# Kernel optimization log

Measured on AMD Instinct MI355X. Metric: run time of the kernel, lower is better.

The kernel has to match this reference:

```python
import jax, jax.numpy as jnp
import numpy as np

C = 64      # extra_msa_channel
AC = 8      # attention_channel (per-head dim)
H = 8       # num_head
LN_EPS = 1e-5


def setup_inputs() -> dict:
    key = jax.random.key(0)
    ks = jax.random.split(key, 8)
    B, S, R = 1, 2048, 384
    msa_act = jax.random.normal(ks[0], (B, S, R, C), dtype=jnp.float32)
    msa_mask = jnp.ones((B, S, R), dtype=jnp.float32)
    # parameters (stored as [in, out] so x @ W matches torch Linear(x) = x @ W.T)
    sq = 1.0 / np.sqrt(C)
    wq = jax.random.normal(ks[1], (C, AC * H), dtype=jnp.float32) * sq
    wk = jax.random.normal(ks[2], (C, AC), dtype=jnp.float32) * sq
    wv = jax.random.normal(ks[3], (C, AC), dtype=jnp.float32) * sq
    wg = jax.random.normal(ks[4], (C, AC * H), dtype=jnp.float32) * sq
    bg = jnp.zeros((AC * H,), dtype=jnp.float32)
    wo = jax.random.normal(ks[5], (AC * H, C), dtype=jnp.float32) / np.sqrt(AC * H)
    bo = jnp.zeros((C,), dtype=jnp.float32)
    ln_scale = jnp.ones((C,), dtype=jnp.float32)
    ln_bias = jnp.zeros((C,), dtype=jnp.float32)
    return {"msa_act": msa_act, "msa_mask": msa_mask, "ln_scale": ln_scale,
            "ln_bias": ln_bias, "wq": wq, "wk": wk, "wv": wv, "wg": wg,
            "bg": bg, "wo": wo, "bo": bo}


def _layer_norm(x, scale, bias):
    mu = jnp.mean(x, axis=-1, keepdims=True)
    var = jnp.mean(jnp.square(x - mu), axis=-1, keepdims=True)
    return (x - mu) * jax.lax.rsqrt(var + LN_EPS) * scale + bias


def reference(msa_act, msa_mask, ln_scale, ln_bias, wq, wk, wv, wg, bg, wo, bo):
    # msa_act: [B, S, R, C] -> [B, R, S, C]; attention runs over S per column R
    act = jnp.swapaxes(msa_act, -2, -3)
    # msa_mask transposed in source but unused in the math
    act = _layer_norm(act, ln_scale, ln_bias)
    B, R, S, _ = act.shape
    # mean-pooled single query per column
    q_avg = jnp.mean(act, axis=-2)                       # [B, R, C]
    q = (q_avg @ wq).reshape(B, R, H, AC) * (AC ** -0.5)  # [B, R, H, ac]
    k = act @ wk                                          # [B, R, S, ac]
    v = act @ wv                                          # [B, R, S, ac]
    gate = jax.nn.sigmoid((act @ wg + bg).reshape(B, R, S, H, AC))
    logits = jnp.einsum('brhc,brsc->brhs', q, k)
    w = jax.nn.softmax(logits, axis=-1)                   # [B, R, H, S]
    out_1d = jnp.einsum('brhs,brsc->brhc', w, v)          # [B, R, H, ac]
    out_1d = out_1d[..., None, :, :] * gate               # [B, R, S, H, ac]
    out = out_1d.reshape(B, R, S, H * AC) @ wo + bo       # [B, R, S, C]
    return jnp.swapaxes(out, -2, -3)                      # [B, S, R, C]
```

## Files before the change

### kernel.cpp

```cpp
#include <hip/hip_runtime.h>

#define S_LEN 2048
#define R_LEN 384
#define C_DIM 64

typedef unsigned short u16;
typedef unsigned int u32;
typedef __attribute__((ext_vector_type(8))) short s8v;
typedef __attribute__((ext_vector_type(4))) float f4v;

__device__ __forceinline__ float bf2f(u16 h) {
    union { u32 u; float f; } c; c.u = ((u32)h) << 16; return c.f;
}
__device__ __forceinline__ u16 f2bf(float f) {
    union { float f; u32 u; } c; c.f = f;
    return (u16)((c.u + 0x7fffu + ((c.u >> 16) & 1u)) >> 16);
}
__device__ __forceinline__ void unpack8(uint4 q, float* o) {
    o[0] = bf2f((u16)(q.x & 0xffffu)); o[1] = bf2f((u16)(q.x >> 16));
    o[2] = bf2f((u16)(q.y & 0xffffu)); o[3] = bf2f((u16)(q.y >> 16));
    o[4] = bf2f((u16)(q.z & 0xffffu)); o[5] = bf2f((u16)(q.z >> 16));
    o[6] = bf2f((u16)(q.w & 0xffffu)); o[7] = bf2f((u16)(q.w >> 16));
}
__device__ __forceinline__ void split8(const float* y, uint4& qh, uint4& ql) {
    u16 h[8]; u16 l[8];
    #pragma unroll
    for (int j = 0; j < 8; ++j) {
        h[j] = f2bf(y[j]);
        l[j] = f2bf(y[j] - bf2f(h[j]));
    }
    qh.x = (u32)h[0] | ((u32)h[1] << 16); qh.y = (u32)h[2] | ((u32)h[3] << 16);
    qh.z = (u32)h[4] | ((u32)h[5] << 16); qh.w = (u32)h[6] | ((u32)h[7] << 16);
    ql.x = (u32)l[0] | ((u32)l[1] << 16); ql.y = (u32)l[2] | ((u32)l[3] << 16);
    ql.z = (u32)l[4] | ((u32)l[5] << 16); ql.w = (u32)l[6] | ((u32)l[7] << 16);
}
__device__ __forceinline__ void load8f(const float* p, float* o) {
    float4 a = *(const float4*)p;
    float4 b = *(const float4*)(p + 4);
    o[0] = a.x; o[1] = a.y; o[2] = a.z; o[3] = a.w;
    o[4] = b.x; o[5] = b.y; o[6] = b.z; o[7] = b.w;
}
#define XS_SWZ(row, bc) ((((int)(row)) << 7) + (((int)(bc)) ^ ((((int)(row)) & 7) << 4)))

__global__ __launch_bounds__(256) void k1_colattn(
    const float* __restrict__ act, const float* __restrict__ lnsp, const float* __restrict__ lnbp,
    const float* __restrict__ wq, const float* __restrict__ wk, const float* __restrict__ wv,
    float* __restrict__ o1g)
{
    __shared__ __align__(16) char smem[32768 + 32768 + 65536 + 8192 + 1024 + 512];
    char* xsh = smem;
    char* xsl = smem + 32768;
    char* kvb = smem + 65536;
    float* scrA = (float*)(smem + 131072);
    float* scrC = (float*)(smem + 139264);
    float* qavg = (float*)(smem + 140288);
    float* qlds = qavg + 64;

    const int t = threadIdx.x;
    const int r = blockIdx.x;
    const int lane = t & 63;
    const int w = t >> 6;
    const int grp = t & 7;
    const int rowb = t >> 3;
    const int n16 = lane & 15;
    const int kgrp = lane >> 4;

    float lns_r[8], lnb_r[8];
    load8f(lnsp + grp * 8, lns_r);
    load8f(lnbp + grp * 8, lnb_r);

    s8v bkv0, bkv1;
    {
        #pragma unroll
        for (int j = 0; j < 8; ++j) {
            int k0 = (kgrp << 3) + j;
            float e0 = (n16 < 8) ? wk[k0 * 8 + n16] : wv[k0 * 8 + (n16 - 8)];
            float e1 = (n16 < 8) ? wk[(k0 + 32) * 8 + n16] : wv[(k0 + 32) * 8 + (n16 - 8)];
            bkv0[j] = (short)f2bf(e0); bkv1[j] = (short)f2bf(e1);
        }
    }

    float qacc[8];
    #pragma unroll
    for (int j = 0; j < 8; ++j) qacc[j] = 0.f;

    for (int ci = 0; ci < 8; ++ci) {
        __syncthreads();
        #pragma unroll
        for (int sub = 0; sub < 8; ++sub) {
            int row = sub * 32 + rowb;
            int s = ci * 256 + row;
            float xf[8];
            load8f(act + ((size_t)s * R_LEN + r) * C_DIM + grp * 8, xf);
            float sum = 0.f, sq = 0.f;
            #pragma unroll
            for (int j = 0; j < 8; ++j) { sum += xf[j]; sq += xf[j] * xf[j]; }
            #pragma unroll
            for (int m = 1; m <= 4; m <<= 1) { sum += __shfl_xor(sum, m); sq += __shfl_xor(sq, m); }
            float mu = sum * (1.f / 64.f);
            float var = sq * (1.f / 64.f) - mu * mu;
            float rstd = rsqrtf(var + 1e-5f);
            float yv[8];
            #pragma unroll
            for (int j = 0; j < 8; ++j) {
                yv[j] = (xf[j] - mu) * rstd * lns_r[j] + lnb_r[j];
                qacc[j] += yv[j];
            }
            uint4 qh, ql; split8(yv, qh, ql);
            *(uint4*)(xsh + XS_SWZ(row, grp * 16)) = qh;
            *(uint4*)(xsl + XS_SWZ(row, grp * 16)) = ql;
        }
        __syncthreads();
        #pragma unroll
        for (int i4 = 0; i4 < 4; ++i4) {
            int tile = w * 4 + i4;
            s8v a0h = *(const s8v*)(xsh + XS_SWZ(tile * 16 + n16, kgrp * 16));
            s8v a1h = *(const s8v*)(xsh + XS_SWZ(tile * 16 + n16, 64 + kgrp * 16));
            s8v a0l = *(const s8v*)(xsl + XS_SWZ(tile * 16 + n16, kgrp * 16));
            s8v a1l = *(const s8v*)(xsl + XS_SWZ(tile * 16 + n16, 64 + kgrp * 16));
            f4v acc = {0.f, 0.f, 0.f, 0.f};
            acc = __builtin_amdgcn_mfma_f32_16x16x32_bf16(a0h, bkv0, acc, 0, 0, 0);
            acc = __builtin_amdgcn_mfma_f32_16x16x32_bf16(a1h, bkv1, acc, 0, 0, 0);
            acc = __builtin_amdgcn_mfma_f32_16x16x32_bf16(a0l, bkv0, acc, 0, 0, 0);
            acc = __builtin_amdgcn_mfma_f32_16x16x32_bf16(a1l, bkv1, acc, 0, 0, 0);
            #pragma unroll
            for (int jj = 0; jj < 4; ++jj) {
                int sg = ci * 256 + tile * 16 + kgrp * 4 + jj;
                int off = sg * 32 + ((n16 * 2) ^ (((sg >> 2) & 1) << 4));
                *(u16*)(kvb + off) = f2bf(acc[jj]);
            }
        }
    }

    #pragma unroll
    for (int j = 0; j < 8; ++j) scrA[t * 8 + j] = qacc[j];
    __syncthreads();
    if (t < 64) {
        float s = 0.f;
        for (int k = 0; k < 32; ++k) s += scrA[((t >> 3) + 8 * k) * 8 + (t & 7)];
        qavg[t] = s * (1.f / (float)S_LEN);
    }
    __syncthreads();
    if (t < 64) {
        float s = 0.f;
        for (int c = 0; c < 64; ++c) s += qavg[c] * wq[c * 64 + t];
        qlds[t] = s * 0.35355339059327373f;
    }
    __syncthreads();
    float q_r[64];
    #pragma unroll
    for (int c = 0; c < 64; ++c) q_r[c] = qlds[c];

    float mx[8];
    #pragma unroll
    for (int h = 0; h < 8; ++h) mx[h] = -1e30f;
    for (int i = 0; i < 8; ++i) {
        int s = i * 256 + t;
        int sw = ((s >> 2) & 1) << 4;
        float kf[8]; unpack8(*(const uint4*)(kvb + s * 32 + sw), kf);
        #pragma unroll
        for (int h = 0; h < 8; ++h) {
            float lg = 0.f;
            #pragma unroll
            for (int a = 0; a < 8; ++a) lg += q_r[h * 8 + a] * kf[a];
            mx[h] = fmaxf(mx[h], lg);
        }
    }
    #pragma unroll
    for (int h = 0; h < 8; ++h) scrA[t * 8 + h] = mx[h];
    __syncthreads();
    for (int st = 128; st >= 1; st >>= 1) {
        if (t < st) {
            #pragma unroll
            for (int h = 0; h < 8; ++h)
                scrA[t * 8 + h] = fmaxf(scrA[t * 8 + h], scrA[(t + st) * 8 + h]);
        }
        __syncthreads();
    }
    float mxf[8];
    #pragma unroll
    for (int h = 0; h < 8; ++h) mxf[h] = scrA[h];
    __syncthreads();

    float sm[8];
    float o1a[64];
    #pragma unroll
    for (int h = 0; h < 8; ++h) sm[h] = 0.f;
    #pragma unroll
    for (int e = 0; e < 64; ++e) o1a[e] = 0.f;
    for (int i = 0; i < 8; ++i) {
        int s = i * 256 + t;
        int sw = ((s >> 2) & 1) << 4;
        float kf[8]; unpack8(*(const uint4*)(kvb + s * 32 + sw), kf);
        float vf[8]; unpack8(*(const uint4*)(kvb + s * 32 + (16 ^ sw)), vf);
        #pragma unroll
        for (int h = 0; h < 8; ++h) {
            float lg = 0.f;
            #pragma unroll
            for (int a = 0; a < 8; ++a) lg += q_r[h * 8 + a] * kf[a];
            float p = __expf(lg - mxf[h]);
            sm[h] += p;
            #pragma unroll
            for (int a = 0; a < 8; ++a) o1a[h * 8 + a] += p * vf[a];
        }
    }
    #pragma unroll
    for (int h = 0; h < 8; ++h) scrA[t * 8 + h] = sm[h];
    __syncthreads();
    for (int st = 128; st >= 1; st >>= 1) {
        if (t < st) {
            #pragma unroll
            for (int h = 0; h < 8; ++h)
                scrA[t * 8 + h] += scrA[(t + st) * 8 + h];
        }
        __syncthreads();
    }
    #pragma unroll
    for (int m = 1; m < 64; m <<= 1) {
        #pragma unroll
        for (int e = 0; e < 64; ++e) o1a[e] += __shfl_xor(o1a[e], m);
    }
    #pragma unroll
    for (int e = 0; e < 64; ++e) if (lane == e) scrC[w * 64 + e] = o1a[e];
    __syncthreads();
    if (t < 64) {
        float v = scrC[t] + scrC[64 + t] + scrC[128 + t] + scrC[192 + t];
        float denom = scrA[t >> 3];
        o1g[r * 64 + t] = v / denom;
    }
}

__global__ __launch_bounds__(256) void k2_gateout(
    const float* __restrict__ act, const float* __restrict__ lnsp, const float* __restrict__ lnbp,
    const float* __restrict__ wg, const float* __restrict__ bgp,
    const float* __restrict__ wo, const float* __restrict__ bop,
    const float* __restrict__ o1g, float* __restrict__ out)
{
    __shared__ __align__(16) char bufH[32768];
    __shared__ __align__(16) char bufL[32768];
    const int t = threadIdx.x;
    const int r = blockIdx.x;
    const int s0 = blockIdx.y * 256;
    const int lane = t & 63;
    const int w = t >> 6;
    const int grp = t & 7;
    const int rowb = t >> 3;
    const int n16 = lane & 15;
    const int kgrp = lane >> 4;

    float lns_r[8], lnb_r[8];
    load8f(lnsp + grp * 8, lns_r);
    load8f(lnbp + grp * 8, lnb_r);

    float o1c[4], bgc[4], boc[4];
    #pragma unroll
    for (int c4 = 0; c4 < 4; ++c4) {
        int col = c4 * 16 + n16;
        o1c[c4] = o1g[r * 64 + col];
        bgc[c4] = bgp[col];
        boc[c4] = bop[col];
    }
    s8v wgf[4][2], wof[4][2];
    #pragma unroll
    for (int c4 = 0; c4 < 4; ++c4) {
        #pragma unroll
        for (int kb = 0; kb < 2; ++kb) {
            #pragma unroll
            for (int j = 0; j < 8; ++j) {
                int k = kb * 32 + kgrp * 8 + j;
                wgf[c4][kb][j] = (short)f2bf(wg[k * 64 + c4 * 16 + n16]);
                wof[c4][kb][j] = (short)f2bf(wo[k * 64 + c4 * 16 + n16]);
            }
        }
    }

    #pragma unroll
    for (int sub = 0; sub < 8; ++sub) {
        int row = sub * 32 + rowb;
        int s = s0 + row;
        float xf[8];
        load8f(act + ((size_t)s * R_LEN + r) * C_DIM + grp * 8, xf);
        float sum = 0.f, sq = 0.f;
        #pragma unroll
        for (int j = 0; j < 8; ++j) { sum += xf[j]; sq += xf[j] * xf[j]; }
        #pragma unroll
        for (int m = 1; m <= 4; m <<= 1) { sum += __shfl_xor(sum, m); sq += __shfl_xor(sq, m); }
        float mu = sum * (1.f / 64.f);
        float var = sq * (1.f / 64.f) - mu * mu;
        float rstd = rsqrtf(var + 1e-5f);
        float yv[8];
        #pragma unroll
        for (int j = 0; j < 8; ++j) yv[j] = (xf[j] - mu) * rstd * lns_r[j] + lnb_r[j];
        uint4 qh, ql; split8(yv, qh, ql);
        *(uint4*)(bufH + XS_SWZ(row, grp * 16)) = qh;
        *(uint4*)(bufL + XS_SWZ(row, grp * 16)) = ql;
    }
    __syncthreads();

    #pragma unroll
    for (int i4 = 0; i4 < 4; ++i4) {
        int tile = w * 4 + i4;
        s8v a0h = *(const s8v*)(bufH + XS_SWZ(tile * 16 + n16, kgrp * 16));
        s8v a1h = *(const s8v*)(bufH + XS_SWZ(tile * 16 + n16, 64 + kgrp * 16));
        s8v a0l = *(const s8v*)(bufL + XS_SWZ(tile * 16 + n16, kgrp * 16));
        s8v a1l = *(const s8v*)(bufL + XS_SWZ(tile * 16 + n16, 64 + kgrp * 16));
        #pragma unroll
        for (int c4 = 0; c4 < 4; ++c4) {
            f4v acc = {0.f, 0.f, 0.f, 0.f};
            acc = __builtin_amdgcn_mfma_f32_16x16x32_bf16(a0h, wgf[c4][0], acc, 0, 0, 0);
            acc = __builtin_amdgcn_mfma_f32_16x16x32_bf16(a1h, wgf[c4][1], acc, 0, 0, 0);
            acc = __builtin_amdgcn_mfma_f32_16x16x32_bf16(a0l, wgf[c4][0], acc, 0, 0, 0);
            acc = __builtin_amdgcn_mfma_f32_16x16x32_bf16(a1l, wgf[c4][1], acc, 0, 0, 0);
            #pragma unroll
            for (int jj = 0; jj < 4; ++jj) {
                float gv = acc[jj] + bgc[c4];
                float sg = 1.f / (1.f + __expf(-gv));
                float tv = sg * o1c[c4];
                u16 th = f2bf(tv);
                u16 tl = f2bf(tv - bf2f(th));
                int row = tile * 16 + kgrp * 4 + jj;
                int off = XS_SWZ(row, (c4 * 16 + n16) * 2);
                *(u16*)(bufH + off) = th;
                *(u16*)(bufL + off) = tl;
            }
        }
    }

    #pragma unroll
    for (int i4 = 0; i4 < 4; ++i4) {
        int tile = w * 4 + i4;
        s8v a0h = *(const s8v*)(bufH + XS_SWZ(tile * 16 + n16, kgrp * 16));
        s8v a1h = *(const s8v*)(bufH + XS_SWZ(tile * 16 + n16, 64 + kgrp * 16));
        s8v a0l = *(const s8v*)(bufL + XS_SWZ(tile * 16 + n16, kgrp * 16));
        s8v a1l = *(const s8v*)(bufL + XS_SWZ(tile * 16 + n16, 64 + kgrp * 16));
        #pragma unroll
        for (int c4 = 0; c4 < 4; ++c4) {
            f4v acc = {0.f, 0.f, 0.f, 0.f};
            acc = __builtin_amdgcn_mfma_f32_16x16x32_bf16(a0h, wof[c4][0], acc, 0, 0, 0);
            acc = __builtin_amdgcn_mfma_f32_16x16x32_bf16(a1h, wof[c4][1], acc, 0, 0, 0);
            acc = __builtin_amdgcn_mfma_f32_16x16x32_bf16(a0l, wof[c4][0], acc, 0, 0, 0);
            acc = __builtin_amdgcn_mfma_f32_16x16x32_bf16(a1l, wof[c4][1], acc, 0, 0, 0);
            #pragma unroll
            for (int jj = 0; jj < 4; ++jj) {
                float ov = acc[jj] + boc[c4];
                u16 oh = f2bf(ov);
                u16 ol = f2bf(ov - bf2f(oh));
                int row = tile * 16 + kgrp * 4 + jj;
                int off = XS_SWZ(row, (c4 * 16 + n16) * 2);
                *(u16*)(bufH + off) = oh;
                *(u16*)(bufL + off) = ol;
            }
        }
    }
    __syncthreads();

    #pragma unroll
    for (int sub = 0; sub < 8; ++sub) {
        int row = sub * 32 + rowb;
        int s = s0 + row;
        float yh[8], yl[8];
        unpack8(*(const uint4*)(bufH + XS_SWZ(row, grp * 16)), yh);
        unpack8(*(const uint4*)(bufL + XS_SWZ(row, grp * 16)), yl);
        float* op = out + ((size_t)s * R_LEN + r) * C_DIM + grp * 8;
        *(float4*)op = make_float4(yh[0] + yl[0], yh[1] + yl[1], yh[2] + yl[2], yh[3] + yl[3]);
        *(float4*)(op + 4) = make_float4(yh[4] + yl[4], yh[5] + yl[5], yh[6] + yl[6], yh[7] + yl[7]);
    }
}

extern "C" void kernel_launch(void* const* d_in, const int* in_sizes, int n_in,
                              void* d_out, int out_size, void* d_ws, size_t ws_size,
                              hipStream_t stream) {
    const float* act = (const float*)d_in[0];
    const float* lns = (const float*)d_in[2];
    const float* lnb = (const float*)d_in[3];
    const float* wq  = (const float*)d_in[4];
    const float* wk  = (const float*)d_in[5];
    const float* wv  = (const float*)d_in[6];
    const float* wg  = (const float*)d_in[7];
    const float* bg  = (const float*)d_in[8];
    const float* wo  = (const float*)d_in[9];
    const float* bo  = (const float*)d_in[10];
    float* out = (float*)d_out;
    float* o1g = (float*)d_ws;

    hipLaunchKernelGGL(k1_colattn, dim3(R_LEN), dim3(256), 0, stream,
                       act, lns, lnb, wq, wk, wv, o1g);
    hipLaunchKernelGGL(k2_gateout, dim3(R_LEN, 8), dim3(256), 0, stream,
                       act, lns, lnb, wg, bg, wo, bo, o1g, out);
}
```

Measured before the change: 605.4 us.

## Split column attention into parallel LN/KV pass, attention pass, and finer gate/out tiles

The per-column k1 kernel, which ran 384 blocks that each walked all 2048 rows serially, is split into three stages. ka_lnkv runs on a 384x16 grid and writes bf16 K/V to workspace, accumulating the column mean via atomics. kb_attn reloads K/V into shared memory for the softmax. The gate/output kernel now uses 128-row tiles with 16 blocks per column and writes fp32 output directly from the MFMA accumulators instead of staging through shared memory. Weights gain a low-bf16 split term, adding two extra MFMAs per tile for accuracy, and a memset plus a K/V round trip through global memory are added costs.

```diff
diff --git a/kernel.cpp b/kernel.cpp
--- a/kernel.cpp
+++ b/kernel.cpp
@@ -40,24 +40,24 @@
     o[0] = a.x; o[1] = a.y; o[2] = a.z; o[3] = a.w;
     o[4] = b.x; o[5] = b.y; o[6] = b.z; o[7] = b.w;
 }
+__device__ __forceinline__ void wsplit(float v, short& h, short& l) {
+    u16 hh = f2bf(v);
+    h = (short)hh;
+    l = (short)f2bf(v - bf2f(hh));
+}
 #define XS_SWZ(row, bc) ((((int)(row)) << 7) + (((int)(bc)) ^ ((((int)(row)) & 7) << 4)))
 
-__global__ __launch_bounds__(256) void k1_colattn(
+__global__ __launch_bounds__(256) void ka_lnkv(
     const float* __restrict__ act, const float* __restrict__ lnsp, const float* __restrict__ lnbp,
-    const float* __restrict__ wq, const float* __restrict__ wk, const float* __restrict__ wv,
-    float* __restrict__ o1g)
+    const float* __restrict__ wk, const float* __restrict__ wv,
+    u16* __restrict__ kv_g, float* __restrict__ qavg_g)
 {
-    __shared__ __align__(16) char smem[32768 + 32768 + 65536 + 8192 + 1024 + 512];
-    char* xsh = smem;
-    char* xsl = smem + 32768;
-    char* kvb = smem + 65536;
-    float* scrA = (float*)(smem + 131072);
-    float* scrC = (float*)(smem + 139264);
-    float* qavg = (float*)(smem + 140288);
-    float* qlds = qavg + 64;
-
+    __shared__ __align__(16) char xs[16384];
+    __shared__ __align__(16) char xsl[16384];
+    __shared__ float scrW[4][64];
     const int t = threadIdx.x;
     const int r = blockIdx.x;
+    const int s0 = blockIdx.y * 128;
     const int lane = t & 63;
     const int w = t >> 6;
     const int grp = t & 7;
@@ -69,84 +69,111 @@
     load8f(lnsp + grp * 8, lns_r);
     load8f(lnbp + grp * 8, lnb_r);
 
-    s8v bkv0, bkv1;
-    {
+    s8v bkv0h, bkv1h, bkv0l, bkv1l;
+    #pragma unroll
+    for (int j = 0; j < 8; ++j) {
+        int k0 = (kgrp << 3) + j;
+        float e0 = (n16 < 8) ? wk[k0 * 8 + n16] : wv[k0 * 8 + (n16 - 8)];
+        float e1 = (n16 < 8) ? wk[(k0 + 32) * 8 + n16] : wv[(k0 + 32) * 8 + (n16 - 8)];
+        short h, l;
+        wsplit(e0, h, l); bkv0h[j] = h; bkv0l[j] = l;
+        wsplit(e1, h, l); bkv1h[j] = h; bkv1l[j] = l;
+    }
+
+    float qacc[8];
+    #pragma unroll
+    for (int j = 0; j < 8; ++j) qacc[j] = 0.f;
+
+    #pragma unroll
+    for (int sub = 0; sub < 4; ++sub) {
+        int row = sub * 32 + rowb;
+        int s = s0 + row;
+        float xf[8];
+        load8f(act + ((size_t)s * R_LEN + r) * C_DIM + grp * 8, xf);
+        float sum = 0.f, sq = 0.f;
+        #pragma unroll
+        for (int j = 0; j < 8; ++j) { sum += xf[j]; sq += xf[j] * xf[j]; }
+        #pragma unroll
+        for (int m = 1; m <= 4; m <<= 1) { sum += __shfl_xor(sum, m); sq += __shfl_xor(sq, m); }
+        float mu = sum * (1.f / 64.f);
+        float var = sq * (1.f / 64.f) - mu * mu;
+        float rstd = rsqrtf(var + 1e-5f);
+        float yv[8];
         #pragma unroll
         for (int j = 0; j < 8; ++j) {
-            int k0 = (kgrp << 3) + j;
-            float e0 = (n16 < 8) ? wk[k0 * 8 + n16] : wv[k0 * 8 + (n16 - 8)];
-            float e1 = (n16 < 8) ? wk[(k0 + 32) * 8 + n16] : wv[(k0 + 32) * 8 + (n16 - 8)];
-            bkv0[j] = (short)f2bf(e0); bkv1[j] = (short)f2bf(e1);
-        }
-    }
-
-    float qacc[8];
-    #pragma unroll
-    for (int j = 0; j < 8; ++j) qacc[j] = 0.f;
-
-    for (int ci = 0; ci < 8; ++ci) {
-        __syncthreads();
-        #pragma unroll
-        for (int sub = 0; sub < 8; ++sub) {
-            int row = sub * 32 + rowb;
-            int s = ci * 256 + row;
-            float xf[8];
-            load8f(act + ((size_t)s * R_LEN + r) * C_DIM + grp * 8, xf);
-            float sum = 0.f, sq = 0.f;
-            #pragma unroll
-            for (int j = 0; j < 8; ++j) { sum += xf[j]; sq += xf[j] * xf[j]; }
-            #pragma unroll
-            for (int m = 1; m <= 4; m <<= 1) { sum += __shfl_xor(sum, m); sq += __shfl_xor(sq, m); }
-            float mu = sum * (1.f / 64.f);
-            float var = sq * (1.f / 64.f) - mu * mu;
-            float rstd = rsqrtf(var + 1e-5f);
-            float yv[8];
-            #pragma unroll
-            for (int j = 0; j < 8; ++j) {
-                yv[j] = (xf[j] - mu) * rstd * lns_r[j] + lnb_r[j];
-                qacc[j] += yv[j];
-            }
-            uint4 qh, ql; split8(yv, qh, ql);
-            *(uint4*)(xsh + XS_SWZ(row, grp * 16)) = qh;
-            *(uint4*)(xsl + XS_SWZ(row, grp * 16)) = ql;
-        }
-        __syncthreads();
-        #pragma unroll
-        for (int i4 = 0; i4 < 4; ++i4) {
-            int tile = w * 4 + i4;
-            s8v a0h = *(const s8v*)(xsh + XS_SWZ(tile * 16 + n16, kgrp * 16));
-            s8v a1h = *(const s8v*)(xsh + XS_SWZ(tile * 16 + n16, 64 + kgrp * 16));
-            s8v a0l = *(const s8v*)(xsl + XS_SWZ(tile * 16 + n16, kgrp * 16));
-            s8v a1l = *(const s8v*)(xsl + XS_SWZ(tile * 16 + n16, 64 + kgrp * 16));
-            f4v acc = {0.f, 0.f, 0.f, 0.f};
-            acc = __builtin_amdgcn_mfma_f32_16x16x32_bf16(a0h, bkv0, acc, 0, 0, 0);
-            acc = __builtin_amdgcn_mfma_f32_16x16x32_bf16(a1h, bkv1, acc, 0, 0, 0);
-            acc = __builtin_amdgcn_mfma_f32_16x16x32_bf16(a0l, bkv0, acc, 0, 0, 0);
-            acc = __builtin_amdgcn_mfma_f32_16x16x32_bf16(a1l, bkv1, acc, 0, 0, 0);
-            #pragma unroll
-            for (int jj = 0; jj < 4; ++jj) {
-                int sg = ci * 256 + tile * 16 + kgrp * 4 + jj;
-                int off = sg * 32 + ((n16 * 2) ^ (((sg >> 2) & 1) << 4));
-                *(u16*)(kvb + off) = f2bf(acc[jj]);
-            }
-        }
-    }
-
-    #pragma unroll
-    for (int j = 0; j < 8; ++j) scrA[t * 8 + j] = qacc[j];
-    __syncthreads();
+            yv[j] = (xf[j] - mu) * rstd * lns_r[j] + lnb_r[j];
+            qacc[j] += yv[j];
+        }
+        uint4 qh, ql; split8(yv, qh, ql);
+        *(uint4*)(xs  + XS_SWZ(row, grp * 16)) = qh;
+        *(uint4*)(xsl + XS_SWZ(row, grp * 16)) = ql;
+    }
+    __syncthreads();
+
+    #pragma unroll
+    for (int i4 = 0; i4 < 2; ++i4) {
+        int tile = w * 2 + i4;
+        s8v a0h = *(const s8v*)(xs  + XS_SWZ(tile * 16 + n16, kgrp * 16));
+        s8v a1h = *(const s8v*)(xs  + XS_SWZ(tile * 16 + n16, 64 + kgrp * 16));
+        s8v a0l = *(const s8v*)(xsl + XS_SWZ(tile * 16 + n16, kgrp * 16));
+        s8v a1l = *(const s8v*)(xsl + XS_SWZ(tile * 16 + n16, 64 + kgrp * 16));
+        f4v acc = {0.f, 0.f, 0.f, 0.f};
+        acc = __builtin_amdgcn_mfma_f32_16x16x32_bf16(a0h, bkv0h, acc, 0, 0, 0);
+        acc = __builtin_amdgcn_mfma_f32_16x16x32_bf16(a1h, bkv1h, acc, 0, 0, 0);
+        acc = __builtin_amdgcn_mfma_f32_16x16x32_bf16(a0l, bkv0h, acc, 0, 0, 0);
+        acc = __builtin_amdgcn_mfma_f32_16x16x32_bf16(a1l, bkv1h, acc, 0, 0, 0);
+        acc = __builtin_amdgcn_mfma_f32_16x16x32_bf16(a0h, bkv0l, acc, 0, 0, 0);
+        acc = __builtin_amdgcn_mfma_f32_16x16x32_bf16(a1h, bkv1l, acc, 0, 0, 0);
+        #pragma unroll
+        for (int jj = 0; jj < 4; ++jj) {
+            int sg = s0 + tile * 16 + kgrp * 4 + jj;
+            kv_g[((size_t)r * S_LEN + sg) * 16 + n16] = f2bf(acc[jj]);
+        }
+    }
+
+    #pragma unroll
+    for (int m = 8; m <= 32; m <<= 1) {
+        #pragma unroll
+        for (int j = 0; j < 8; ++j) qacc[j] += __shfl_xor(qacc[j], m);
+    }
+    if (lane < 8) {
+        #pragma unroll
+        for (int j = 0; j < 8; ++j) scrW[w][lane * 8 + j] = qacc[j];
+    }
+    __syncthreads();
+    if (t < 64) {
+        float v = scrW[0][t] + scrW[1][t] + scrW[2][t] + scrW[3][t];
+        atomicAdd(&qavg_g[r * 64 + t], v);
+    }
+}
+
+__global__ __launch_bounds__(256) void kb_attn(
+    const u16* __restrict__ kv_g, const float* __restrict__ qavg_g,
+    const float* __restrict__ wq, float* __restrict__ o1g)
+{
+    __shared__ __align__(16) char kvb[65536];
+    __shared__ float scrA[256 * 8];
+    __shared__ float scrC[4 * 64];
+    __shared__ float qlds[64];
+    const int t = threadIdx.x;
+    const int r = blockIdx.x;
+    const int lane = t & 63;
+    const int w = t >> 6;
+
+    #pragma unroll
+    for (int i = 0; i < 16; ++i) {
+        int f = i * 256 + t;
+        int s = f >> 1, half = f & 1;
+        uint4 q = *(const uint4*)((const char*)kv_g + (size_t)r * 65536 + (size_t)f * 16);
+        *(uint4*)(kvb + s * 32 + ((half << 4) ^ (((s >> 2) & 1) << 4))) = q;
+    }
     if (t < 64) {
         float s = 0.f;
-        for (int k = 0; k < 32; ++k) s += scrA[((t >> 3) + 8 * k) * 8 + (t & 7)];
-        qavg[t] = s * (1.f / (float)S_LEN);
-    }
-    __syncthreads();
-    if (t < 64) {
-        float s = 0.f;
-        for (int c = 0; c < 64; ++c) s += qavg[c] * wq[c * 64 + t];
-        qlds[t] = s * 0.35355339059327373f;
-    }
-    __syncthreads();
+        for (int c = 0; c < 64; ++c) s += qavg_g[r * 64 + c] * wq[c * 64 + t];
+        qlds[t] = s * (0.35355339059327373f / (float)S_LEN);
+    }
+    __syncthreads();
+
     float q_r[64];
     #pragma unroll
     for (int c = 0; c < 64; ++c) q_r[c] = qlds[c];
@@ -225,22 +252,21 @@
     __syncthreads();
     if (t < 64) {
         float v = scrC[t] + scrC[64 + t] + scrC[128 + t] + scrC[192 + t];
-        float denom = scrA[t >> 3];
-        o1g[r * 64 + t] = v / denom;
-    }
-}
-
-__global__ __launch_bounds__(256) void k2_gateout(
+        o1g[r * 64 + t] = v / scrA[t >> 3];
+    }
+}
+
+__global__ __launch_bounds__(256) void kc_gateout(
     const float* __restrict__ act, const float* __restrict__ lnsp, const float* __restrict__ lnbp,
     const float* __restrict__ wg, const float* __restrict__ bgp,
     const float* __restrict__ wo, const float* __restrict__ bop,
     const float* __restrict__ o1g, float* __restrict__ out)
 {
-    __shared__ __align__(16) char bufH[32768];
-    __shared__ __align__(16) char bufL[32768];
+    __shared__ __align__(16) char bufH[16384];
+    __shared__ __align__(16) char bufL[16384];
     const int t = threadIdx.x;
     const int r = blockIdx.x;
-    const int s0 = blockIdx.y * 256;
+    const int s0 = blockIdx.y * 128;
     const int lane = t & 63;
     const int w = t >> 6;
     const int grp = t & 7;
@@ -260,22 +286,9 @@
         bgc[c4] = bgp[col];
         boc[c4] = bop[col];
     }
-    s8v wgf[4][2], wof[4][2];
-    #pragma unroll
-    for (int c4 = 0; c4 < 4; ++c4) {
-        #pragma unroll
-        for (int kb = 0; kb < 2; ++kb) {
-            #pragma unroll
-            for (int j = 0; j < 8; ++j) {
-                int k = kb * 32 + kgrp * 8 + j;
-                wgf[c4][kb][j] = (short)f2bf(wg[k * 64 + c4 * 16 + n16]);
-                wof[c4][kb][j] = (short)f2bf(wo[k * 64 + c4 * 16 + n16]);
-            }
-        }
-    }
-
-    #pragma unroll
-    for (int sub = 0; sub < 8; ++sub) {
+
+    #pragma unroll
+    for (int sub = 0; sub < 4; ++sub) {
         int row = sub * 32 + rowb;
         int s = s0 + row;
         float xf[8];
@@ -297,73 +310,92 @@
     }
     __syncthreads();
 
-    #pragma unroll
-    for (int i4 = 0; i4 < 4; ++i4) {
-        int tile = w * 4 + i4;
-        s8v a0h = *(const s8v*)(bufH + XS_SWZ(tile * 16 + n16, kgrp * 16));
-        s8v a1h = *(const s8v*)(bufH + XS_SWZ(tile * 16 + n16, 64 + kgrp * 16));
-        s8v a0l = *(const s8v*)(bufL + XS_SWZ(tile * 16 + n16, kgrp * 16));
-        s8v a1l = *(const s8v*)(bufL + XS_SWZ(tile * 16 + n16, 64 + kgrp * 16));
+    {
+        s8v wgh[4][2], wgl[4][2];
         #pragma unroll
         for (int c4 = 0; c4 < 4; ++c4) {
-            f4v acc = {0.f, 0.f, 0.f, 0.f};
-            acc = __builtin_amdgcn_mfma_f32_16x16x32_bf16(a0h, wgf[c4][0], acc, 0, 0, 0);
-            acc = __builtin_amdgcn_mfma_f32_16x16x32_bf16(a1h, wgf[c4][1], acc, 0, 0, 0);
-            acc = __builtin_amdgcn_mfma_f32_16x16x32_bf16(a0l, wgf[c4][0], acc, 0, 0, 0);
-            acc = __builtin_amdgcn_mfma_f32_16x16x32_bf16(a1l, wgf[c4][1], acc, 0, 0, 0);
-            #pragma unroll
-            for (int jj = 0; jj < 4; ++jj) {
-                float gv = acc[jj] + bgc[c4];
-                float sg = 1.f / (1.f + __expf(-gv));
-                float tv = sg * o1c[c4];
-                u16 th = f2bf(tv);
-                u16 tl = f2bf(tv - bf2f(th));
-                int row = tile * 16 + kgrp * 4 + jj;
-                int off = XS_SWZ(row, (c4 * 16 + n16) * 2);
-                *(u16*)(bufH + off) = th;
-                *(u16*)(bufL + off) = tl;
+            #pragma unroll
+            for (int kb = 0; kb < 2; ++kb) {
+                #pragma unroll
+                for (int j = 0; j < 8; ++j) {
+                    int k = kb * 32 + kgrp * 8 + j;
+                    short h, l;
+                    wsplit(wg[k * 64 + c4 * 16 + n16], h, l);
+                    wgh[c4][kb][j] = h; wgl[c4][kb][j] = l;
+                }
             }
         }
-    }
-
-    #pragma unroll
-    for (int i4 = 0; i4 < 4; ++i4) {
-        int tile = w * 4 + i4;
-        s8v a0h = *(const s8v*)(bufH + XS_SWZ(tile * 16 + n16, kgrp * 16));
-        s8v a1h = *(const s8v*)(bufH + XS_SWZ(tile * 16 + n16, 64 + kgrp * 16));
-        s8v a0l = *(const s8v*)(bufL + XS_SWZ(tile * 16 + n16, kgrp * 16));
-        s8v a1l = *(const s8v*)(bufL + XS_SWZ(tile * 16 + n16, 64 + kgrp * 16));
+        #pragma unroll
+        for (int i4 = 0; i4 < 2; ++i4) {
+            int tile = w * 2 + i4;
+            s8v a0h = *(const s8v*)(bufH + XS_SWZ(tile * 16 + n16, kgrp * 16));
+            s8v a1h = *(const s8v*)(bufH + XS_SWZ(tile * 16 + n16, 64 + kgrp * 16));
+            s8v a0l = *(const s8v*)(bufL + XS_SWZ(tile * 16 + n16, kgrp * 16));
+            s8v a1l = *(const s8v*)(bufL + XS_SWZ(tile * 16 + n16, 64 + kgrp * 16));
+            #pragma unroll
+            for (int c4 = 0; c4 < 4; ++c4) {
+                f4v acc = {0.f, 0.f, 0.f, 0.f};
+                acc = __builtin_amdgcn_mfma_f32_16x16x32_bf16(a0h, wgh[c4][0], acc, 0, 0, 0);
+                acc = __builtin_amdgcn_mfma_f32_16x16x32_bf16(a1h, wgh[c4][1], acc, 0, 0, 0);
+                acc = __builtin_amdgcn_mfma_f32_16x16x32_bf16(a0l, wgh[c4][0], acc, 0, 0, 0);
+                acc = __builtin_amdgcn_mfma_f32_16x16x32_bf16(a1l, wgh[c4][1], acc, 0, 0, 0);
+                acc = __builtin_amdgcn_mfma_f32_16x16x32_bf16(a0h, wgl[c4][0], acc, 0, 0, 0);
+                acc = __builtin_amdgcn_mfma_f32_16x16x32_bf16(a1h, wgl[c4][1], acc, 0, 0, 0);
+                #pragma unroll
+                for (int jj = 0; jj < 4; ++jj) {
+                    float gv = acc[jj] + bgc[c4];
+                    float sg = 1.f / (1.f + __expf(-gv));
+                    float tv = sg * o1c[c4];
+                    u16 th = f2bf(tv);
+                    u16 tl = f2bf(tv - bf2f(th));
+                    int row = tile * 16 + kgrp * 4 + jj;
+                    int off = XS_SWZ(row, (c4 * 16 + n16) * 2);
+                    *(u16*)(bufH + off) = th;
+                    *(u16*)(bufL + off) = tl;
+                }
+            }
+        }
+    }
+
+    {
+        s8v woh[4][2], wol[4][2];
         #pragma unroll
         for (int c4 = 0; c4 < 4; ++c4) {
-            f4v acc = {0.f, 0.f, 0.f, 0.f};
-            acc = __builtin_amdgcn_mfma_f32_16x16x32_bf16(a0h, wof[c4][0], acc, 0, 0, 0);
-            acc = __builtin_amdgcn_mfma_f32_16x16x32_bf16(a1h, wof[c4][1], acc, 0, 0, 0);
-            acc = __builtin_amdgcn_mfma_f32_16x16x32_bf16(a0l, wof[c4][0], acc, 0, 0, 0);
-            acc = __builtin_amdgcn_mfma_f32_16x16x32_bf16(a1l, wof[c4][1], acc, 0, 0, 0);
-            #pragma unroll
-            for (int jj = 0; jj < 4; ++jj) {
-                float ov = acc[jj] + boc[c4];
-                u16 oh = f2bf(ov);
-                u16 ol = f2bf(ov - bf2f(oh));
-                int row = tile * 16 + kgrp * 4 + jj;
-                int off = XS_SWZ(row, (c4 * 16 + n16) * 2);
-                *(u16*)(bufH + off) = oh;
-                *(u16*)(bufL + off) = ol;
+            #pragma unroll
+            for (int kb = 0; kb < 2; ++kb) {
+                #pragma unroll
+                for (int j = 0; j < 8; ++j) {
+                    int k = kb * 32 + kgrp * 8 + j;
+                    short h, l;
+                    wsplit(wo[k * 64 + c4 * 16 + n16], h, l);
+                    woh[c4][kb][j] = h; wol[c4][kb][j] = l;
+                }
             }
         }
-    }
-    __syncthreads();
-
-    #pragma unroll
-    for (int sub = 0; sub < 8; ++sub) {
-        int row = sub * 32 + rowb;
-        int s = s0 + row;
-        float yh[8], yl[8];
-        unpack8(*(const uint4*)(bufH + XS_SWZ(row, grp * 16)), yh);
-        unpack8(*(const uint4*)(bufL + XS_SWZ(row, grp * 16)), yl);
-        float* op = out + ((size_t)s * R_LEN + r) * C_DIM + grp * 8;
-        *(float4*)op = make_float4(yh[0] + yl[0], yh[1] + yl[1], yh[2] + yl[2], yh[3] + yl[3]);
-        *(float4*)(op + 4) = make_float4(yh[4] + yl[4], yh[5] + yl[5], yh[6] + yl[6], yh[7] + yl[7]);
+        #pragma unroll
+        for (int i4 = 0; i4 < 2; ++i4) {
+            int tile = w * 2 + i4;
+            s8v a0h = *(const s8v*)(bufH + XS_SWZ(tile * 16 + n16, kgrp * 16));
+            s8v a1h = *(const s8v*)(bufH + XS_SWZ(tile * 16 + n16, 64 + kgrp * 16));
+            s8v a0l = *(const s8v*)(bufL + XS_SWZ(tile * 16 + n16, kgrp * 16));
+            s8v a1l = *(const s8v*)(bufL + XS_SWZ(tile * 16 + n16, 64 + kgrp * 16));
+            #pragma unroll
+            for (int c4 = 0; c4 < 4; ++c4) {
+                f4v acc = {0.f, 0.f, 0.f, 0.f};
+                acc = __builtin_amdgcn_mfma_f32_16x16x32_bf16(a0h, woh[c4][0], acc, 0, 0, 0);
+                acc = __builtin_amdgcn_mfma_f32_16x16x32_bf16(a1h, woh[c4][1], acc, 0, 0, 0);
+                acc = __builtin_amdgcn_mfma_f32_16x16x32_bf16(a0l, woh[c4][0], acc, 0, 0, 0);
+                acc = __builtin_amdgcn_mfma_f32_16x16x32_bf16(a1l, woh[c4][1], acc, 0, 0, 0);
+                acc = __builtin_amdgcn_mfma_f32_16x16x32_bf16(a0h, wol[c4][0], acc, 0, 0, 0);
+                acc = __builtin_amdgcn_mfma_f32_16x16x32_bf16(a1h, wol[c4][1], acc, 0, 0, 0);
+                #pragma unroll
+                for (int jj = 0; jj < 4; ++jj) {
+                    int row = tile * 16 + kgrp * 4 + jj;
+                    int s = s0 + row;
+                    out[((size_t)s * R_LEN + r) * C_DIM + c4 * 16 + n16] = acc[jj] + boc[c4];
+                }
+            }
+        }
     }
 }
 
@@ -381,10 +413,16 @@
     const float* wo  = (const float*)d_in[9];
     const float* bo  = (const float*)d_in[10];
     float* out = (float*)d_out;
-    float* o1g = (float*)d_ws;
-
-    hipLaunchKernelGGL(k1_colattn, dim3(R_LEN), dim3(256), 0, stream,
-                       act, lns, lnb, wq, wk, wv, o1g);
-    hipLaunchKernelGGL(k2_gateout, dim3(R_LEN, 8), dim3(256), 0, stream,
+
+    float* o1g    = (float*)d_ws;
+    float* qavg_g = (float*)((char*)d_ws + 98304);
+    u16*   kv_g   = (u16*)((char*)d_ws + 196608);
+
+    hipMemsetAsync(qavg_g, 0, 98304, stream);
+    hipLaunchKernelGGL(ka_lnkv, dim3(R_LEN, 16), dim3(256), 0, stream,
+                       act, lns, lnb, wk, wv, kv_g, qavg_g);
+    hipLaunchKernelGGL(kb_attn, dim3(R_LEN), dim3(256), 0, stream,
+                       kv_g, qavg_g, wq, o1g);
+    hipLaunchKernelGGL(kc_gateout, dim3(R_LEN, 16), dim3(256), 0, stream,
                        act, lns, lnb, wg, bg, wo, bo, o1g, out);
 }
```

After: 631.8 us. +4.4%, slower.
